# Performance work log

Measured on AMD Instinct MI355X. Metric: run time of the kernel, lower is better.

## Reference

```python
import jax, jax.numpy as jnp
import numpy as np

T_SEG = 8  # n_segment


def _layer_norm(x, eps=1e-5):
    # F.layer_norm over last dim, no affine (torch default eps=1e-5)
    mu = x.mean(-1, keepdims=True)
    var = ((x - mu) ** 2).mean(-1, keepdims=True)
    return (x - mu) / jnp.sqrt(var + eps)


def setup_inputs() -> dict:
    key = jax.random.key(0)
    k1, k2, k3 = jax.random.split(key, 3)
    B, T, C, H, W = 8, T_SEG, 512, 56, 56
    R = C // 4  # rsize = in_channels // n_div
    x = jax.random.normal(k1, (B * T, C, H, W), jnp.float32)
    W_down = jax.random.normal(k2, (R, C), jnp.float32) / np.sqrt(C).astype(np.float32)
    b_down = jnp.zeros((R,), jnp.float32)
    W_up = jax.random.normal(k3, (C, R), jnp.float32) / np.sqrt(R).astype(np.float32)
    b_up = jnp.zeros((C,), jnp.float32)
    return {"x": x, "W_down": W_down, "b_down": b_down, "W_up": W_up, "b_up": b_up}


def reference(x, W_down, b_down, W_up, b_up):
    t = T_SEG
    shortcut = x
    # conv_down: 1x1 conv == per-pixel GEMM
    h = jnp.einsum('bchw,oc->bohw', x, W_down) + b_down[None, :, None, None]
    bt, c, H, W = h.shape
    b = bt // t

    def to_attn(z):  # (b t) c h w -> (b h w) t c
        return z.reshape(b, t, c, H, W).transpose(0, 3, 4, 1, 2).reshape(b * H * W, t, c)

    def from_attn(z):  # (b h w) t c -> (b t) c h w
        return z.reshape(b, H, W, t, c).transpose(0, 3, 4, 1, 2).reshape(bt, c, H, W)

    # LayerNorm over channel dim (last dim of attn layout)
    xn = from_attn(_layer_norm(to_attn(h)))

    # Motion: rearrange to (b, t, c, h, w), shift-left along dim 3 (h), subtract
    z = xn.reshape(b, t, c, H, W)
    shifted = jnp.concatenate([z[:, :, :, 1:], jnp.zeros_like(z[:, :, :, :1])], axis=3)
    xn = (shifted - z).reshape(bt, c, H, W)

    # raw bmm self-attention with q = k = v
    q = to_attn(xn)  # ((b h w), t, c)
    scores = jax.nn.softmax(
        jnp.einsum('btc,bsc->bts', q, q) / jnp.sqrt(jnp.float32(c)), axis=-1)
    attn = jnp.einsum('bts,bsc->btc', scores, q)

    h = from_attn(attn) + h  # residual inside attention block

    # conv_up + sigmoid gate + residual
    up = jnp.einsum('bchw,oc->bohw', h, W_up) + b_up[None, :, None, None]
    gate = jax.nn.sigmoid(up)
    return gate * shortcut + shortcut
```

## Files before the change

kernel.cpp:

```cpp
#include <hip/hip_runtime.h>
#include <cstdint>
#include <cstddef>

#define HW   3136
#define WROW 56
#define CIN  512
#define RMID 128
#define HWQ  196

typedef unsigned int  u32;
typedef unsigned short u16;
typedef __attribute__((ext_vector_type(8))) short s16x8;
typedef __attribute__((ext_vector_type(4))) float f32x4;

__device__ __forceinline__ u16 f2bf(float f) {
    u32 u = __float_as_uint(f);
    u32 r = u + 0x7fffu + ((u >> 16) & 1u);
    return (u16)(r >> 16);
}
__device__ __forceinline__ float bf2f(u32 bits16) {
    return __uint_as_float(bits16 << 16);
}
__device__ __forceinline__ u32 pk2(float a, float b) {
    return (u32)f2bf(a) | ((u32)f2bf(b) << 16);
}

__global__ __launch_bounds__(256) void kprep(
    const float* __restrict__ Wd, const float* __restrict__ Wu,
    u16* __restrict__ wdf, u16* __restrict__ wuf)
{
    const int t = blockIdx.x * 256 + threadIdx.x;
    const int l = t & 63, g = t >> 6;
    const int lo = l & 15, hi = l >> 4;
    const float* src;
    u16* dst;
    if (g < 128) {
        const int s = g >> 3, m = g & 7;
        src = Wd + (size_t)(m * 16 + lo) * CIN + s * 32 + hi * 8;
        dst = wdf + (size_t)t * 8;
    } else {
        const int g2 = g - 128;
        const int mt = g2 >> 2, s = g2 & 3;
        src = Wu + (size_t)(mt * 16 + lo) * RMID + s * 32 + hi * 8;
        dst = wuf + (size_t)(t - 8192) * 8;
    }
    float4 a = *(const float4*)src;
    float4 b = *(const float4*)(src + 4);
    uint4 o;
    o.x = pk2(a.x, a.y); o.y = pk2(a.z, a.w);
    o.z = pk2(b.x, b.y); o.w = pk2(b.z, b.w);
    *(uint4*)dst = o;
}

__global__ __launch_bounds__(256) void k1_down_ln(
    const float* __restrict__ x, const u16* __restrict__ wdf,
    const float* __restrict__ bd, u16* __restrict__ hd,
    float* __restrict__ st)
{
    __shared__ u16 xl[128 * 40];

    const int tid  = threadIdx.x;
    const int lane = tid & 63, w = tid >> 6;
    const int h = blockIdx.x;
    const int slot = h >> 3;
    const int bt = (h & 7) * 8 + slot / 25;
    const int px0 = (slot % 25) * 128;
    const int b = bt >> 3, t = bt & 7;

    const int pxp2 = px0 + 2 * lane;
    const int pxa = (pxp2 > HW - 2) ? (HW - 2) : pxp2;
    const float* xb = x + (size_t)bt * CIN * HW + pxa;

    const int p16 = lane & 15, lg = lane >> 4;

    f32x4 acc[8][2];
    const f32x4 zz = {0.f, 0.f, 0.f, 0.f};
#pragma unroll
    for (int m = 0; m < 8; ++m) { acc[m][0] = zz; acc[m][1] = zz; }

    for (int s = 0; s < 16; ++s) {
        const float* xs = xb + (size_t)(s * 32 + w * 8) * HW;
        float2 v[8];
#pragma unroll
        for (int j = 0; j < 8; ++j)
            v[j] = *(const float2*)(xs + (size_t)j * HW);
        uint4 pkA, pkB;
        pkA.x = pk2(v[0].x, v[1].x); pkA.y = pk2(v[2].x, v[3].x);
        pkA.z = pk2(v[4].x, v[5].x); pkA.w = pk2(v[6].x, v[7].x);
        pkB.x = pk2(v[0].y, v[1].y); pkB.y = pk2(v[2].y, v[3].y);
        pkB.z = pk2(v[4].y, v[5].y); pkB.w = pk2(v[6].y, v[7].y);
        *(uint4*)&xl[(size_t)(2 * lane)     * 40 + w * 8] = pkA;
        *(uint4*)&xl[(size_t)(2 * lane + 1) * 40 + w * 8] = pkB;
        __syncthreads();
        s16x8 bf0 = *(const s16x8*)&xl[(w * 32 +      p16) * 40 + lg * 8];
        s16x8 bf1 = *(const s16x8*)&xl[(w * 32 + 16 + p16) * 40 + lg * 8];
#pragma unroll
        for (int m = 0; m < 8; ++m) {
            s16x8 af = *(const s16x8*)(wdf + ((size_t)((s * 8 + m) * 64 + lane)) * 8);
            acc[m][0] = __builtin_amdgcn_mfma_f32_16x16x32_bf16(af, bf0, acc[m][0], 0, 0, 0);
            acc[m][1] = __builtin_amdgcn_mfma_f32_16x16x32_bf16(af, bf1, acc[m][1], 0, 0, 0);
        }
        __syncthreads();
    }

#pragma unroll
    for (int n = 0; n < 2; ++n) {
        const int hwpx = px0 + w * 32 + n * 16 + p16;
        const bool ok = hwpx < HW;
        float sum = 0.f, sq = 0.f;
        const size_t hbase = ((size_t)(b * HW + (ok ? hwpx : 0)) * 8 + t) * 128 + lg * 4;
#pragma unroll
        for (int m = 0; m < 8; ++m) {
            float4 bv = *(const float4*)(bd + m * 16 + lg * 4);
            float v0 = acc[m][n].x + bv.x;
            float v1 = acc[m][n].y + bv.y;
            float v2 = acc[m][n].z + bv.z;
            float v3 = acc[m][n].w + bv.w;
            sum += v0 + v1 + v2 + v3;
            sq  += v0*v0 + v1*v1 + v2*v2 + v3*v3;
            if (ok) {
                ushort4 o;
                o.x = f2bf(v0); o.y = f2bf(v1); o.z = f2bf(v2); o.w = f2bf(v3);
                *(ushort4*)(hd + hbase + m * 16) = o;
            }
        }
        sum += __shfl_xor(sum, 16); sum += __shfl_xor(sum, 32);
        sq  += __shfl_xor(sq, 16);  sq  += __shfl_xor(sq, 32);
        if (ok && lg == 0) {
            float mu  = sum * (1.f / 128.f);
            float var = sq  * (1.f / 128.f) - mu * mu;
            float2 s2 = make_float2(mu, rsqrtf(var + 1e-5f));
            *(float2*)(st + ((size_t)(b * HW + hwpx) * 8 + t) * 2) = s2;
        }
    }
}

__global__ __launch_bounds__(256) void k2a_attn(
    const u16* __restrict__ hd, const float* __restrict__ st,
    u16* __restrict__ h2f)
{
    __shared__ float ql[4][8 * 132];
    __shared__ float pl[4][8][9];

    const int tid = threadIdx.x, wid = tid >> 6, lane = tid & 63;
    const int P = blockIdx.x * 4 + wid;
    const int b = P / HW;
    const int hw = P - b * HW;
    const int hrow = hw / WROW;
    const bool hasnext = hrow < (WROW - 1);

    const u16* cur = hd + (size_t)P * 1024;
    const int tq = lane >> 3, cbase = (lane & 7) * 16;

    uint4 c0 = *(const uint4*)(cur + tq * 128 + cbase);
    uint4 c1 = *(const uint4*)(cur + tq * 128 + cbase + 8);
    float2 ms = *(const float2*)(st + ((size_t)P * 8 + tq) * 2);

    float hv[16];
    hv[0]=bf2f(c0.x&0xffff); hv[1]=bf2f(c0.x>>16); hv[2]=bf2f(c0.y&0xffff); hv[3]=bf2f(c0.y>>16);
    hv[4]=bf2f(c0.z&0xffff); hv[5]=bf2f(c0.z>>16); hv[6]=bf2f(c0.w&0xffff); hv[7]=bf2f(c0.w>>16);
    hv[8]=bf2f(c1.x&0xffff); hv[9]=bf2f(c1.x>>16); hv[10]=bf2f(c1.y&0xffff); hv[11]=bf2f(c1.y>>16);
    hv[12]=bf2f(c1.z&0xffff); hv[13]=bf2f(c1.z>>16); hv[14]=bf2f(c1.w&0xffff); hv[15]=bf2f(c1.w>>16);

    float qv[16];
    if (hasnext) {
        const u16* nx = cur + (size_t)WROW * 1024;
        uint4 n0 = *(const uint4*)(nx + tq * 128 + cbase);
        uint4 n1 = *(const uint4*)(nx + tq * 128 + cbase + 8);
        float2 mn = *(const float2*)(st + ((size_t)(P + WROW) * 8 + tq) * 2);
        float nv[16];
        nv[0]=bf2f(n0.x&0xffff); nv[1]=bf2f(n0.x>>16); nv[2]=bf2f(n0.y&0xffff); nv[3]=bf2f(n0.y>>16);
        nv[4]=bf2f(n0.z&0xffff); nv[5]=bf2f(n0.z>>16); nv[6]=bf2f(n0.w&0xffff); nv[7]=bf2f(n0.w>>16);
        nv[8]=bf2f(n1.x&0xffff); nv[9]=bf2f(n1.x>>16); nv[10]=bf2f(n1.y&0xffff); nv[11]=bf2f(n1.y>>16);
        nv[12]=bf2f(n1.z&0xffff); nv[13]=bf2f(n1.z>>16); nv[14]=bf2f(n1.w&0xffff); nv[15]=bf2f(n1.w>>16);
#pragma unroll
        for (int i = 0; i < 16; ++i)
            qv[i] = (nv[i] - mn.x) * mn.y - (hv[i] - ms.x) * ms.y;
    } else {
#pragma unroll
        for (int i = 0; i < 16; ++i)
            qv[i] = -(hv[i] - ms.x) * ms.y;
    }

    float* qrow = &ql[wid][tq * 132 + cbase];
#pragma unroll
    for (int i = 0; i < 4; ++i)
        *(float4*)(qrow + i * 4) = make_float4(qv[4*i], qv[4*i+1], qv[4*i+2], qv[4*i+3]);
    __syncthreads();

    const int tt = lane >> 3, ss = lane & 7;
    const float* qt = &ql[wid][tt * 132];
    const float* qs = &ql[wid][ss * 132];
    float dot = 0.f;
#pragma unroll 8
    for (int c4 = 0; c4 < 32; ++c4) {
        float4 a4 = *(const float4*)(qt + c4 * 4);
        float4 g4 = *(const float4*)(qs + c4 * 4);
        dot += a4.x*g4.x + a4.y*g4.y + a4.z*g4.z + a4.w*g4.w;
    }
    dot *= 0.08838834764831845f;
    float mx = dot;
    mx = fmaxf(mx, __shfl_xor(mx, 1));
    mx = fmaxf(mx, __shfl_xor(mx, 2));
    mx = fmaxf(mx, __shfl_xor(mx, 4));
    float e = __expf(dot - mx);
    float sm = e;
    sm += __shfl_xor(sm, 1); sm += __shfl_xor(sm, 2); sm += __shfl_xor(sm, 4);
    pl[wid][tt][ss] = e / sm;
    __syncthreads();

    float at[16];
#pragma unroll
    for (int i = 0; i < 16; ++i) at[i] = hv[i];
#pragma unroll
    for (int s = 0; s < 8; ++s) {
        float p = pl[wid][tq][s];
        const float* qsr = &ql[wid][s * 132 + cbase];
#pragma unroll
        for (int i4 = 0; i4 < 4; ++i4) {
            float4 q4 = *(const float4*)(qsr + i4 * 4);
            at[4*i4+0] += p * q4.x; at[4*i4+1] += p * q4.y;
            at[4*i4+2] += p * q4.z; at[4*i4+3] += p * q4.w;
        }
    }

    const int hwq = hw >> 4, pp = hw & 15;
    const size_t base = ((((size_t)(b * 8 + tq) * HWQ + hwq) * 16 + (cbase >> 3)) * 16 + pp) * 8;
    uint4 o0, o1;
    o0.x = pk2(at[0], at[1]);  o0.y = pk2(at[2], at[3]);
    o0.z = pk2(at[4], at[5]);  o0.w = pk2(at[6], at[7]);
    o1.x = pk2(at[8], at[9]);  o1.y = pk2(at[10], at[11]);
    o1.z = pk2(at[12], at[13]); o1.w = pk2(at[14], at[15]);
    *(uint4*)(h2f + base) = o0;
    *(uint4*)(h2f + base + 128) = o1;
}

__global__ __launch_bounds__(64, 4) void k2b_up_out(
    const u16* __restrict__ h2f, const u16* __restrict__ wuf,
    const float* __restrict__ bu, const float* __restrict__ x,
    float* __restrict__ out)
{
    __shared__ float sl[16 * 68];

    const int lane = threadIdx.x;
    const int h = blockIdx.x;
    const int slot = h >> 3;
    const int bt = (h & 7) * 8 + (slot >> 7);
    const int oc = (slot & 127) >> 2;
    const int q  = slot & 3;
    const int p16 = lane & 15, lg = lane >> 4;

    s16x8 wf[4];
#pragma unroll
    for (int s = 0; s < 4; ++s)
        wf[s] = *(const s16x8*)(wuf + ((size_t)((oc * 4 + s) * 64 + lane)) * 8);

    float bvr[4];
#pragma unroll
    for (int i = 0; i < 4; ++i) bvr[i] = bu[oc * 16 + i * 4 + lg];

    const u16* bp0 = h2f + (size_t)bt * HWQ * 2048;
    const size_t xrow = (size_t)bt * CIN * HW + (size_t)(oc * 16) * HW;

    const int ng = (q == 0) ? 13 : 12;
    for (int it = 0; it < ng; ++it) {
        const int g = (it < 12) ? (it * 4 + q) : 48;
        const int px0 = g * 64;

        float4 xv[4];
#pragma unroll
        for (int i = 0; i < 4; ++i)
            xv[i] = *(const float4*)(x + xrow + (size_t)(i * 4 + lg) * HW + px0 + p16 * 4);

#pragma unroll
        for (int tt = 0; tt < 4; ++tt) {
            const u16* bp = bp0 + (size_t)(g * 4 + tt) * 2048;
            f32x4 a = {0.f, 0.f, 0.f, 0.f};
#pragma unroll
            for (int s = 0; s < 4; ++s) {
                s16x8 af = *(const s16x8*)(bp + ((size_t)((s * 4 + lg) * 16 + p16)) * 8);
                a = __builtin_amdgcn_mfma_f32_16x16x32_bf16(af, wf[s], a, 0, 0, 0);
            }
            *(f32x4*)&sl[p16 * 68 + tt * 16 + lg * 4] = a;
        }

#pragma unroll
        for (int i = 0; i < 4; ++i) {
            const int ol = i * 4 + lg;
            f32x4 a4 = *(const f32x4*)&sl[ol * 68 + p16 * 4];
            const size_t off = xrow + (size_t)ol * HW + px0 + p16 * 4;
            float4 rr;
            rr.x = xv[i].x * (1.f + 1.f / (1.f + __expf(-(a4.x + bvr[i]))));
            rr.y = xv[i].y * (1.f + 1.f / (1.f + __expf(-(a4.y + bvr[i]))));
            rr.z = xv[i].z * (1.f + 1.f / (1.f + __expf(-(a4.z + bvr[i]))));
            rr.w = xv[i].w * (1.f + 1.f / (1.f + __expf(-(a4.w + bvr[i]))));
            *(float4*)(out + off) = rr;
        }
    }
}

extern "C" void kernel_launch(void* const* d_in, const int* in_sizes, int n_in,
                              void* d_out, int out_size, void* d_ws, size_t ws_size,
                              hipStream_t stream)
{
    (void)in_sizes; (void)n_in; (void)out_size; (void)ws_size;
    const float* x  = (const float*)d_in[0];
    const float* Wd = (const float*)d_in[1];
    const float* bd = (const float*)d_in[2];
    const float* Wu = (const float*)d_in[3];
    const float* bu = (const float*)d_in[4];
    float* out = (float*)d_out;

    char* wsp = (char*)d_ws;
    u16*  hd  = (u16*)wsp;                 wsp += 51380224;
    u16*  h2f = (u16*)wsp;                 wsp += 51380224;
    float* st = (float*)wsp;               wsp += 1605632;
    u16*  wdf = (u16*)wsp;                 wsp += 131072;
    u16*  wuf = (u16*)wsp;                 wsp += 131072;

    kprep     <<<dim3(64),   256, 0, stream>>>(Wd, Wu, wdf, wuf);
    k1_down_ln<<<dim3(1600), 256, 0, stream>>>(x, wdf, bd, hd, st);
    k2a_attn  <<<dim3(6272), 256, 0, stream>>>(hd, st, h2f);
    k2b_up_out<<<dim3(8192), 64,  0, stream>>>(h2f, wuf, bu, x, out);
}
```

Baseline: 420.5 us.

## Double-buffer k1 LDS staging, remap k2a blocks, merge k2b waves into 256-thread blocks

k1 now double-buffers the bf16 LDS tile, so global loads for the next channel slice are issued before the MFMAs on the current one, and one barrier per iteration is enough. k2a remaps block indices with an XCD-style interleave (h&7) so neighbouring pixels land on the same die. k2b packs the four wave quarters of the same (bt, oc) into one 256-thread block, with per-wave LDS and a higher occupancy hint. Together these aim to hide load latency and improve L2 locality and scheduling, at the cost of extra LDS and register pressure.

```diff
diff --git a/kernel.cpp b/kernel.cpp
--- a/kernel.cpp
+++ b/kernel.cpp
@@ -57,7 +57,7 @@
     const float* __restrict__ bd, u16* __restrict__ hd,
     float* __restrict__ st)
 {
-    __shared__ u16 xl[128 * 40];
+    __shared__ u16 xl[2][128 * 40];
 
     const int tid  = threadIdx.x;
     const int lane = tid & 63, w = tid >> 6;
@@ -73,33 +73,43 @@
 
     const int p16 = lane & 15, lg = lane >> 4;
 
-    f32x4 acc[8][2];
-    const f32x4 zz = {0.f, 0.f, 0.f, 0.f};
-#pragma unroll
-    for (int m = 0; m < 8; ++m) { acc[m][0] = zz; acc[m][1] = zz; }
-
-    for (int s = 0; s < 16; ++s) {
+    float2 v[8];
+    auto loads = [&](int s) {
         const float* xs = xb + (size_t)(s * 32 + w * 8) * HW;
-        float2 v[8];
 #pragma unroll
         for (int j = 0; j < 8; ++j)
             v[j] = *(const float2*)(xs + (size_t)j * HW);
+    };
+    auto packw = [&](int buf) {
         uint4 pkA, pkB;
         pkA.x = pk2(v[0].x, v[1].x); pkA.y = pk2(v[2].x, v[3].x);
         pkA.z = pk2(v[4].x, v[5].x); pkA.w = pk2(v[6].x, v[7].x);
         pkB.x = pk2(v[0].y, v[1].y); pkB.y = pk2(v[2].y, v[3].y);
         pkB.z = pk2(v[4].y, v[5].y); pkB.w = pk2(v[6].y, v[7].y);
-        *(uint4*)&xl[(size_t)(2 * lane)     * 40 + w * 8] = pkA;
-        *(uint4*)&xl[(size_t)(2 * lane + 1) * 40 + w * 8] = pkB;
-        __syncthreads();
-        s16x8 bf0 = *(const s16x8*)&xl[(w * 32 +      p16) * 40 + lg * 8];
-        s16x8 bf1 = *(const s16x8*)&xl[(w * 32 + 16 + p16) * 40 + lg * 8];
+        *(uint4*)&xl[buf][(size_t)(2 * lane)     * 40 + w * 8] = pkA;
+        *(uint4*)&xl[buf][(size_t)(2 * lane + 1) * 40 + w * 8] = pkB;
+    };
+
+    f32x4 acc[8][2];
+    const f32x4 zz = {0.f, 0.f, 0.f, 0.f};
+#pragma unroll
+    for (int m = 0; m < 8; ++m) { acc[m][0] = zz; acc[m][1] = zz; }
+
+    loads(0); packw(0);
+    __syncthreads();
+
+    for (int s = 0; s < 16; ++s) {
+        if (s < 15) loads(s + 1);
+        const u16* xbuf = xl[s & 1];
+        s16x8 bf0 = *(const s16x8*)&xbuf[(w * 32 +      p16) * 40 + lg * 8];
+        s16x8 bf1 = *(const s16x8*)&xbuf[(w * 32 + 16 + p16) * 40 + lg * 8];
 #pragma unroll
         for (int m = 0; m < 8; ++m) {
             s16x8 af = *(const s16x8*)(wdf + ((size_t)((s * 8 + m) * 64 + lane)) * 8);
             acc[m][0] = __builtin_amdgcn_mfma_f32_16x16x32_bf16(af, bf0, acc[m][0], 0, 0, 0);
             acc[m][1] = __builtin_amdgcn_mfma_f32_16x16x32_bf16(af, bf1, acc[m][1], 0, 0, 0);
         }
+        if (s < 15) packw((s + 1) & 1);
         __syncthreads();
     }
 
@@ -143,7 +153,8 @@
     __shared__ float pl[4][8][9];
 
     const int tid = threadIdx.x, wid = tid >> 6, lane = tid & 63;
-    const int P = blockIdx.x * 4 + wid;
+    const int h = blockIdx.x;
+    const int P = ((h & 7) * 784 + (h >> 3)) * 4 + wid;
     const int b = P / HW;
     const int hw = P - b * HW;
     const int hrow = hw / WROW;
@@ -235,20 +246,21 @@
     *(uint4*)(h2f + base + 128) = o1;
 }
 
-__global__ __launch_bounds__(64, 4) void k2b_up_out(
+__global__ __launch_bounds__(256, 8) void k2b_up_out(
     const u16* __restrict__ h2f, const u16* __restrict__ wuf,
     const float* __restrict__ bu, const float* __restrict__ x,
     float* __restrict__ out)
 {
-    __shared__ float sl[16 * 68];
-
-    const int lane = threadIdx.x;
+    __shared__ float sl[4][16 * 68];
+
+    const int tid = threadIdx.x, lane = tid & 63, w = tid >> 6;
     const int h = blockIdx.x;
     const int slot = h >> 3;
-    const int bt = (h & 7) * 8 + (slot >> 7);
-    const int oc = (slot & 127) >> 2;
-    const int q  = slot & 3;
+    const int bt = (h & 7) * 8 + (slot >> 5);
+    const int oc = slot & 31;
+    const int q  = w;
     const int p16 = lane & 15, lg = lane >> 4;
+    float* slw = sl[w];
 
     s16x8 wf[4];
 #pragma unroll
@@ -281,13 +293,13 @@
                 s16x8 af = *(const s16x8*)(bp + ((size_t)((s * 4 + lg) * 16 + p16)) * 8);
                 a = __builtin_amdgcn_mfma_f32_16x16x32_bf16(af, wf[s], a, 0, 0, 0);
             }
-            *(f32x4*)&sl[p16 * 68 + tt * 16 + lg * 4] = a;
+            *(f32x4*)&slw[p16 * 68 + tt * 16 + lg * 4] = a;
         }
 
 #pragma unroll
         for (int i = 0; i < 4; ++i) {
             const int ol = i * 4 + lg;
-            f32x4 a4 = *(const f32x4*)&sl[ol * 68 + p16 * 4];
+            f32x4 a4 = *(const f32x4*)&slw[ol * 68 + p16 * 4];
             const size_t off = xrow + (size_t)ol * HW + px0 + p16 * 4;
             float4 rr;
             rr.x = xv[i].x * (1.f + 1.f / (1.f + __expf(-(a4.x + bvr[i]))));
@@ -321,5 +333,5 @@
     kprep     <<<dim3(64),   256, 0, stream>>>(Wd, Wu, wdf, wuf);
     k1_down_ln<<<dim3(1600), 256, 0, stream>>>(x, wdf, bd, hd, st);
     k2a_attn  <<<dim3(6272), 256, 0, stream>>>(hd, st, h2f);
-    k2b_up_out<<<dim3(8192), 64,  0, stream>>>(h2f, wuf, bu, x, out);
-}
+    k2b_up_out<<<dim3(2048), 256, 0, stream>>>(h2f, wuf, bu, x, out);
+}
```

After: 415.4 us. About the same (-1.2%).
